# Kernel optimization log

Hardware: AMD Instinct MI355X
Metric: run time of the kernel (lower is better)

## Reference

```python
import jax, jax.numpy as jnp
import numpy as np

N_EMBD = 2048
N_HEAD = 16
N_KV_HEAD = 4
HD = N_EMBD // N_HEAD  # 128
B, T = 1, 4096
EPS = 1e-6


def apply_rope(x, cos, sin):
    # x: [B,T,H,hd]; cos/sin: [T,1,hd//2]
    hd = x.shape[-1] // 2
    x1, x2 = x[..., :hd], x[..., hd:]
    y1 = x1 * cos + x2 * sin
    y2 = x2 * cos - x1 * sin
    return jnp.concatenate((y1, y2), axis=-1).astype(x.dtype)


def rms_norm(x, eps=EPS):
    return x * jax.lax.rsqrt(jnp.mean(jnp.square(x), axis=-1, keepdims=True) + eps)


def setup_inputs() -> dict:
    key = jax.random.key(0)
    ks = jax.random.split(key, 7)
    s = 0.02
    return {
        "x": jax.random.normal(ks[0], (B, T, N_EMBD), dtype=jnp.float32),
        "cos": jax.random.normal(ks[1], (T, 1, HD // 2), dtype=jnp.float32),
        "sin": jax.random.normal(ks[2], (T, 1, HD // 2), dtype=jnp.float32),
        "wq": jax.random.normal(ks[3], (N_EMBD, N_HEAD * HD), dtype=jnp.float32) * s,
        "wk": jax.random.normal(ks[4], (N_EMBD, N_KV_HEAD * HD), dtype=jnp.float32) * s,
        "wv": jax.random.normal(ks[5], (N_EMBD, N_KV_HEAD * HD), dtype=jnp.float32) * s,
        "wo": jax.random.normal(ks[6], (N_EMBD, N_EMBD), dtype=jnp.float32) * s,
    }


def reference(x, cos, sin, wq, wk, wv, wo):
    Bb, Tt, C = x.shape
    q = (x @ wq).reshape(Bb, Tt, N_HEAD, HD)
    k = (x @ wk).reshape(Bb, Tt, N_KV_HEAD, HD)
    v = (x @ wv).reshape(Bb, Tt, N_KV_HEAD, HD)
    q = rms_norm(apply_rope(q, cos, sin))
    k = rms_norm(apply_rope(k, cos, sin))
    g = N_HEAD // N_KV_HEAD
    if g > 1:
        k = jnp.repeat(k, g, axis=2)  # [B,T,H,hd]
        v = jnp.repeat(v, g, axis=2)
    scale = 1.0 / jnp.sqrt(jnp.float32(HD))
    # scores: [B,H,T,S]
    scores = jnp.einsum("bthd,bshd->bhts", q, k) * scale
    causal = jnp.tril(jnp.ones((Tt, Tt), dtype=bool))
    scores = jnp.where(causal, scores, jnp.finfo(scores.dtype).min)
    attn = jax.nn.softmax(scores, axis=-1)
    y = jnp.einsum("bhts,bshd->bthd", attn, v).reshape(Bb, Tt, C)
    return y @ wo
```

## Files before the change

kernel.cpp:

```cpp
#include <hip/hip_runtime.h>

#define T_SEQ 4096
#define C_EMB 2048
#define NH 16
#define NKV 4
#define HD 128

typedef short bf16x8 __attribute__((ext_vector_type(8)));
typedef float f32x4 __attribute__((ext_vector_type(4)));
typedef unsigned short u16x4 __attribute__((ext_vector_type(4)));

__device__ inline unsigned short f2bf(float f) {
    unsigned int u = __float_as_uint(f);
    unsigned int r = (u + 0x7FFFu + ((u >> 16) & 1u)) >> 16;
    return (unsigned short)r;
}

__device__ __forceinline__ void async_cp16(const unsigned short* g, unsigned short* l) {
    __builtin_amdgcn_global_load_lds((const __attribute__((address_space(1))) unsigned int*)g,
                                     (__attribute__((address_space(3))) unsigned int*)l,
                                     16, 0, 0);
}

__global__ __launch_bounds__(256) void cvt_bf16(const float* __restrict__ in,
                                                unsigned short* __restrict__ out, int n) {
    int i = (blockIdx.x * 256 + threadIdx.x) * 4;
    if (i >= n) return;
    float4 f = *(const float4*)(&in[i]);
    u16x4 o;
    o.x = f2bf(f.x); o.y = f2bf(f.y); o.z = f2bf(f.z); o.w = f2bf(f.w);
    *(u16x4*)(&out[i]) = o;
}

__global__ __launch_bounds__(256) void transpose_all(const float* __restrict__ wq,
                                                     const float* __restrict__ wk,
                                                     const float* __restrict__ wv,
                                                     const float* __restrict__ wo,
                                                     unsigned short* __restrict__ wqkvT,
                                                     unsigned short* __restrict__ woT) {
    __shared__ float tile[32][33];
    int z = blockIdx.z;
    const float* in;
    unsigned short* out;
    int ld_in;
    if (z == 0)      { in = wq; out = wqkvT;                         ld_in = 2048; }
    else if (z == 1) { in = wk; out = wqkvT + (size_t)2048 * 2048;   ld_in = 512;  }
    else if (z == 2) { in = wv; out = wqkvT + (size_t)2560 * 2048;   ld_in = 512;  }
    else             { in = wo; out = woT;                           ld_in = 2048; }
    if ((z == 1 || z == 2) && blockIdx.x >= 16) return;

    int x = blockIdx.x * 32 + threadIdx.x;
    for (int i = threadIdx.y; i < 32; i += 8) {
        int y = blockIdx.y * 32 + i;
        tile[i][threadIdx.x] = in[(size_t)y * ld_in + x];
    }
    __syncthreads();
    int xo = blockIdx.y * 32 + threadIdx.x;
    for (int i = threadIdx.y; i < 32; i += 8) {
        int yo = blockIdx.x * 32 + i;
        out[(size_t)yo * 2048 + xo] = f2bf(tile[threadIdx.x][i]);
    }
}

__global__ __launch_bounds__(256, 3) void gemm_qkv(const unsigned short* __restrict__ A,
                                                   const unsigned short* __restrict__ Bt,
                                                   const float* __restrict__ cosb,
                                                   const float* __restrict__ sinb,
                                                   unsigned short* __restrict__ Qn,
                                                   unsigned short* __restrict__ Kn,
                                                   unsigned short* __restrict__ Vt) {
    __shared__ __align__(16) unsigned short As[3][128 * 32];
    __shared__ __align__(16) unsigned short Bs[3][128 * 32];
    const int K = 2048;
    int t = threadIdx.x;
    int w = t >> 6, lane = t & 63;
    int ln = lane & 15, q = lane >> 4;
    int wm = w * 32;

    int d = blockIdx.y * 24 + blockIdx.x;
    int xcd = d & 7, l = d >> 3;
    int lx = l % 12, ly = l / 12;
    int bx = (xcd & 1) * 12 + lx;
    int by = (xcd >> 1) * 8 + ly;
    int m0 = by * 128, n0 = bx * 128;

    f32x4 acc[2][8] = {};

    int r0 = t >> 2, c0 = (t & 3) ^ ((t >> 4) & 3);
    int L1 = 256 + t;
    int r1 = L1 >> 2, c1 = (L1 & 3) ^ ((L1 >> 4) & 3);
    const unsigned short* a0 = &A[(size_t)(m0 + r0) * K + c0 * 8];
    const unsigned short* a1 = &A[(size_t)(m0 + r1) * K + c1 * 8];
    const unsigned short* b0 = &Bt[(size_t)(n0 + r0) * K + c0 * 8];
    const unsigned short* b1 = &Bt[(size_t)(n0 + r1) * K + c1 * 8];

    auto stage = [&](int b, int k0) {
        async_cp16(a0 + k0, &As[b][w * 512]);
        async_cp16(a1 + k0, &As[b][2048 + w * 512]);
        async_cp16(b0 + k0, &Bs[b][w * 512]);
        async_cp16(b1 + k0, &Bs[b][2048 + w * 512]);
    };

    stage(0, 0);
    stage(1, 32);

    int bc = 0;
    for (int it = 0; it < 64; ++it) {
        if (it < 63) asm volatile("s_waitcnt vmcnt(4)" ::: "memory");
        else         asm volatile("s_waitcnt vmcnt(0)" ::: "memory");
        __builtin_amdgcn_s_barrier();
        __builtin_amdgcn_sched_barrier(0);
        if (it < 62) {
            int bn = bc + 2; if (bn >= 3) bn -= 3;
            stage(bn, (it + 2) * 32);
        }
        int cs = (q ^ ((ln >> 2) & 3)) * 8;
        bf16x8 af[2], bfr[8];
#pragma unroll
        for (int i = 0; i < 2; ++i) af[i] = *(const bf16x8*)(&As[bc][(wm + i * 16 + ln) * 32 + cs]);
#pragma unroll
        for (int j = 0; j < 8; ++j) bfr[j] = *(const bf16x8*)(&Bs[bc][(j * 16 + ln) * 32 + cs]);
#pragma unroll
        for (int i = 0; i < 2; ++i)
#pragma unroll
            for (int j = 0; j < 8; ++j)
                acc[i][j] = __builtin_amdgcn_mfma_f32_16x16x32_bf16(af[i], bfr[j], acc[i][j], 0, 0, 0);
        bc = (bc == 2) ? 0 : bc + 1;
    }

    if (n0 < 2560) {
        bool isQ = (n0 < 2048);
        int h = isQ ? (n0 >> 7) : ((n0 - 2048) >> 7);
#pragma unroll
        for (int i = 0; i < 2; ++i)
#pragma unroll
            for (int r = 0; r < 4; ++r) {
                int row = m0 + wm + i * 16 + q * 4 + r;
                float y1[4], y2[4];
                float ss = 0.0f;
#pragma unroll
                for (int j = 0; j < 4; ++j) {
                    float a = acc[i][j][r];
                    float b = acc[i][j + 4][r];
                    float cc = cosb[row * 64 + j * 16 + ln];
                    float sv = sinb[row * 64 + j * 16 + ln];
                    y1[j] = a * cc + b * sv;
                    y2[j] = b * cc - a * sv;
                    ss += y1[j] * y1[j] + y2[j] * y2[j];
                }
                ss += __shfl_xor(ss, 1);
                ss += __shfl_xor(ss, 2);
                ss += __shfl_xor(ss, 4);
                ss += __shfl_xor(ss, 8);
                float rv = rsqrtf(ss * (1.0f / 128.0f) + 1e-6f);
                if (isQ) {
                    float s = rv * (0.08838834764831845f * 1.4426950408889634f);
                    unsigned short* ob = Qn + (size_t)row * 2048 + h * 128;
#pragma unroll
                    for (int j = 0; j < 4; ++j) {
                        ob[j * 16 + ln] = f2bf(y1[j] * s);
                        ob[64 + j * 16 + ln] = f2bf(y2[j] * s);
                    }
                } else {
                    unsigned short* ob = Kn + (size_t)row * 512 + h * 128;
#pragma unroll
                    for (int j = 0; j < 4; ++j) {
                        ob[j * 16 + ln] = f2bf(y1[j] * rv);
                        ob[64 + j * 16 + ln] = f2bf(y2[j] * rv);
                    }
                }
            }
    } else {
        int v0 = n0 - 2560;
        unsigned short* sm = &As[0][0];
#pragma unroll
        for (int half = 0; half < 2; ++half) {
            __syncthreads();
#pragma unroll
            for (int i = 0; i < 2; ++i)
#pragma unroll
                for (int jj = 0; jj < 4; ++jj) {
                    int j = half * 4 + jj;
                    int cc = jj * 16 + ln;
                    int rr = wm + i * 16 + q * 4;
                    u16x4 pk;
                    pk.x = f2bf(acc[i][j][0]); pk.y = f2bf(acc[i][j][1]);
                    pk.z = f2bf(acc[i][j][2]); pk.w = f2bf(acc[i][j][3]);
                    *(u16x4*)(&sm[cc * 136 + rr]) = pk;
                }
            __syncthreads();
            int vtr = t >> 2, mseg = (t & 3) * 32;
            unsigned short* dst = Vt + (size_t)(v0 + half * 64 + vtr) * 4096 + m0 + mseg;
            const unsigned short* src = &sm[vtr * 136 + mseg];
            *(int4*)(dst)      = *(const int4*)(src);
            *(int4*)(dst + 8)  = *(const int4*)(src + 8);
            *(int4*)(dst + 16) = *(const int4*)(src + 16);
            *(int4*)(dst + 24) = *(const int4*)(src + 24);
        }
    }
}

__global__ __launch_bounds__(512, 2) void gemm_bt_v12(const unsigned short* __restrict__ A,
                                                      const unsigned short* __restrict__ Bt,
                                                      float* __restrict__ C, int M, int N, int K) {
    __shared__ __align__(16) unsigned short As[2][256 * 64];
    __shared__ __align__(16) unsigned short Bs[2][128 * 64];
    int t = threadIdx.x;
    int w = t >> 6, lane = t & 63;
    int ln = lane & 15, q = lane >> 4;
    int wr = w >> 1, wc = w & 1;
    int m0 = blockIdx.y * 256, n0 = blockIdx.x * 128;

    f32x4 acc[4][4] = {};

    const unsigned short* ab[4];
    const unsigned short* bb[2];
#pragma unroll
    for (int s = 0; s < 4; ++s) {
        int L = s * 512 + t;
        int r = L >> 3;
        int c = (L & 7) ^ (r & 7);
        ab[s] = &A[(size_t)(m0 + r) * K + c * 8];
    }
#pragma unroll
    for (int s = 0; s < 2; ++s) {
        int L = s * 512 + t;
        int r = L >> 3;
        int c = (L & 7) ^ (r & 7);
        bb[s] = &Bt[(size_t)(n0 + r) * K + c * 8];
    }

    auto stage = [&](int b, int k0) {
#pragma unroll
        for (int s = 0; s < 4; ++s) async_cp16(ab[s] + k0, &As[b][s * 4096 + w * 512]);
#pragma unroll
        for (int s = 0; s < 2; ++s) async_cp16(bb[s] + k0, &Bs[b][s * 4096 + w * 512]);
    };

    stage(0, 0);
    asm volatile("s_waitcnt vmcnt(0)" ::: "memory");
    __builtin_amdgcn_s_barrier();

    int buf = 0;
    for (int it = 0; it < 32; ++it) {
        if (it < 31) stage(buf ^ 1, (it + 1) * 64);
#pragma unroll
        for (int kk = 0; kk < 2; ++kk) {
            bf16x8 bfr[4];
#pragma unroll
            for (int j = 0; j < 4; ++j) {
                int row = wc * 64 + j * 16 + ln;
                bfr[j] = *(const bf16x8*)(&Bs[buf][row * 64 + (((kk * 4 + q) ^ (row & 7)) * 8)]);
            }
#pragma unroll
            for (int i = 0; i < 4; ++i) {
                int row = wr * 64 + i * 16 + ln;
                bf16x8 a = *(const bf16x8*)(&As[buf][row * 64 + (((kk * 4 + q) ^ (row & 7)) * 8)]);
#pragma unroll
                for (int j = 0; j < 4; ++j)
                    acc[i][j] = __builtin_amdgcn_mfma_f32_16x16x32_bf16(a, bfr[j], acc[i][j], 0, 0, 0);
            }
        }
        asm volatile("s_waitcnt vmcnt(0)" ::: "memory");
        __builtin_amdgcn_s_barrier();
        buf ^= 1;
    }

#pragma unroll
    for (int i = 0; i < 4; ++i)
#pragma unroll
        for (int j = 0; j < 4; ++j)
#pragma unroll
            for (int r = 0; r < 4; ++r) {
                int row = m0 + wr * 64 + i * 16 + q * 4 + r;
                int col = n0 + wc * 64 + j * 16 + ln;
                C[(size_t)row * N + col] = acc[i][j][r];
            }
}

__global__ __launch_bounds__(256) void flash_attn(const unsigned short* __restrict__ Qn,
                                                  const unsigned short* __restrict__ Kn,
                                                  const unsigned short* __restrict__ Vt,
                                                  unsigned short* __restrict__ Ao) {
    __shared__ __align__(16) unsigned short Ks[2][64 * 128];
    __shared__ __align__(16) unsigned short Vs[2][128 * 64];
    __shared__ __align__(16) unsigned short Pl[4][16 * 72];

    int pairi = blockIdx.x;
    int h = blockIdx.y;
    int kvh = h >> 2;
    int t = threadIdx.x;
    int w = t >> 6, lane = t & 63;
    int ln = lane & 15, q = lane >> 4;

    int nA = 64 - pairi;
    int bq = 63 - pairi;
    int wq0 = bq * 64 + w * 16;

    bf16x8 qf[4];
    {
        const unsigned short* qb = Qn + (size_t)(wq0 + ln) * 2048 + h * 128;
#pragma unroll
        for (int kc = 0; kc < 4; ++kc) qf[kc] = *(const bf16x8*)(qb + kc * 32 + q * 8);
    }

    f32x4 o[8] = {};
    f32x4 l_p = {0.f, 0.f, 0.f, 0.f};

    const unsigned short* kbase[4];
    const unsigned short* vbase[4];
#pragma unroll
    for (int s = 0; s < 4; ++s) {
        int L = s * 256 + t;
        int key = L >> 4;
        int ck = (L & 15) ^ (key & 15);
        kbase[s] = Kn + (size_t)key * 512 + kvh * 128 + ck * 8;
        int hd = L >> 3;
        int cv = (L & 7) ^ (hd & 7);
        vbase[s] = Vt + (size_t)(kvh * 128 + hd) * 4096 + cv * 8;
    }

#pragma unroll
    for (int s = 0; s < 4; ++s) async_cp16(kbase[s], &Ks[0][s * 2048 + w * 512]);
#pragma unroll
    for (int s = 0; s < 4; ++s) async_cp16(vbase[s], &Vs[0][s * 2048 + w * 512]);

    for (int it = 0; it < 65; ++it) {
        __syncthreads();

        int nxt = it + 1;
        if (nxt < 65) {
            int nkt = (nxt < nA) ? nxt * 64 : (nxt - nA) * 64;
            size_t koff = (size_t)nkt * 512;
            unsigned short* kd = Ks[nxt & 1];
            unsigned short* vd = Vs[nxt & 1];
#pragma unroll
            for (int s = 0; s < 4; ++s) async_cp16(kbase[s] + koff, kd + s * 2048 + w * 512);
#pragma unroll
            for (int s = 0; s < 4; ++s) async_cp16(vbase[s] + nkt, vd + s * 2048 + w * 512);
        }

        if (it == nA) {
#pragma unroll
            for (int r = 0; r < 4; ++r) {
                float lsum = l_p[r];
                lsum += __shfl_xor(lsum, 1);
                lsum += __shfl_xor(lsum, 2);
                lsum += __shfl_xor(lsum, 4);
                lsum += __shfl_xor(lsum, 8);
                float inv = 1.0f / lsum;
                int row = wq0 + q * 4 + r;
                unsigned short* ob = Ao + (size_t)row * 2048 + h * 128;
#pragma unroll
                for (int f = 0; f < 8; ++f) ob[f * 16 + ln] = f2bf(o[f][r] * inv);
            }
            bq = pairi;
            wq0 = bq * 64 + w * 16;
            const unsigned short* qb = Qn + (size_t)(wq0 + ln) * 2048 + h * 128;
#pragma unroll
            for (int kc = 0; kc < 4; ++kc) qf[kc] = *(const bf16x8*)(qb + kc * 32 + q * 8);
#pragma unroll
            for (int f = 0; f < 8; ++f) o[f] = (f32x4){0.f, 0.f, 0.f, 0.f};
            l_p = (f32x4){0.f, 0.f, 0.f, 0.f};
        }

        int kt0 = (it < nA) ? it * 64 : (it - nA) * 64;
        const unsigned short* kb = Ks[it & 1];
        const unsigned short* vb = Vs[it & 1];

        f32x4 sA[4] = {{-16.6f, -16.6f, -16.6f, -16.6f}, {-16.6f, -16.6f, -16.6f, -16.6f},
                       {-16.6f, -16.6f, -16.6f, -16.6f}, {-16.6f, -16.6f, -16.6f, -16.6f}};
        __builtin_amdgcn_s_setprio(1);
#pragma unroll
        for (int jt = 0; jt < 4; ++jt) {
            int key = jt * 16 + ln;
#pragma unroll
            for (int kc = 0; kc < 4; ++kc) {
                int cs = ((kc * 4 + q) ^ ln) * 8;
                bf16x8 kf = *(const bf16x8*)(&kb[key * 128 + cs]);
                sA[jt] = __builtin_amdgcn_mfma_f32_16x16x32_bf16(qf[kc], kf, sA[jt], 0, 0, 0);
            }
        }
        __builtin_amdgcn_s_setprio(0);
        if (kt0 + 63 > wq0) {
#pragma unroll
            for (int jt = 0; jt < 4; ++jt)
#pragma unroll
                for (int r = 0; r < 4; ++r) {
                    int key = kt0 + jt * 16 + ln;
                    int row = wq0 + q * 4 + r;
                    if (key > row) sA[jt][r] = -3e38f;
                }
        }
#pragma unroll
        for (int r = 0; r < 4; ++r) {
            int prow = (q * 4 + r) * 72;
#pragma unroll
            for (int jt = 0; jt < 4; ++jt) {
                float p = __builtin_amdgcn_exp2f(sA[jt][r]);
                Pl[w][prow + jt * 16 + ln] = (unsigned short)(__float_as_uint(p) >> 16);
                l_p[r] += p;
            }
        }

        __builtin_amdgcn_s_setprio(1);
#pragma unroll
        for (int ks = 0; ks < 2; ++ks) {
            bf16x8 pa = *(const bf16x8*)(&Pl[w][ln * 72 + ks * 32 + q * 8]);
            int cs = ((ks * 4 + q) ^ (ln & 7)) * 8;
#pragma unroll
            for (int f = 0; f < 8; ++f) {
                bf16x8 vf = *(const bf16x8*)(&vb[(f * 16 + ln) * 64 + cs]);
                o[f] = __builtin_amdgcn_mfma_f32_16x16x32_bf16(pa, vf, o[f], 0, 0, 0);
            }
        }
        __builtin_amdgcn_s_setprio(0);
    }
#pragma unroll
    for (int r = 0; r < 4; ++r) {
        float lsum = l_p[r];
        lsum += __shfl_xor(lsum, 1);
        lsum += __shfl_xor(lsum, 2);
        lsum += __shfl_xor(lsum, 4);
        lsum += __shfl_xor(lsum, 8);
        float inv = 1.0f / lsum;
        int row = wq0 + q * 4 + r;
        unsigned short* ob = Ao + (size_t)row * 2048 + h * 128;
#pragma unroll
        for (int f = 0; f < 8; ++f) ob[f * 16 + ln] = f2bf(o[f][r] * inv);
    }
}

extern "C" void kernel_launch(void* const* d_in, const int* in_sizes, int n_in,
                              void* d_out, int out_size, void* d_ws, size_t ws_size,
                              hipStream_t stream) {
    const float* x    = (const float*)d_in[0];
    const float* cosb = (const float*)d_in[1];
    const float* sinb = (const float*)d_in[2];
    const float* wq   = (const float*)d_in[3];
    const float* wk   = (const float*)d_in[4];
    const float* wv   = (const float*)d_in[5];
    const float* wo   = (const float*)d_in[6];
    float* out = (float*)d_out;

    char* ws = (char*)d_ws;
    unsigned short* xb    = (unsigned short*)ws;
    unsigned short* wqkvT = xb    + (size_t)4096 * 2048;
    unsigned short* woT   = wqkvT + (size_t)3072 * 2048;
    unsigned short* Qn    = woT   + (size_t)2048 * 2048;
    unsigned short* Kn    = Qn    + (size_t)4096 * 2048;
    unsigned short* Vt    = Kn    + (size_t)4096 * 512;
    unsigned short* Ao    = Vt    + (size_t)512 * 4096;

    cvt_bf16<<<(4096 * 2048 / 4 + 255) / 256, 256, 0, stream>>>(x, xb, 4096 * 2048);
    transpose_all<<<dim3(64, 64, 4), dim3(32, 8), 0, stream>>>(wq, wk, wv, wo, wqkvT, woT);
    gemm_qkv<<<dim3(24, 32), 256, 0, stream>>>(xb, wqkvT, cosb, sinb, Qn, Kn, Vt);
    flash_attn<<<dim3(32, 16), 256, 0, stream>>>(Qn, Kn, Vt, Ao);
    gemm_bt_v12<<<dim3(16, 16), 512, 0, stream>>>(Ao, woT, out, 4096, 2048, 2048);
}
```

Baseline: 352.6 us.

## Split flash-attention warps into 2x2 query/key groups with cross-warp reduction

```diff
diff --git a/kernel.cpp b/kernel.cpp
--- a/kernel.cpp
+++ b/kernel.cpp
@@ -284,7 +284,8 @@
                                                   unsigned short* __restrict__ Ao) {
     __shared__ __align__(16) unsigned short Ks[2][64 * 128];
     __shared__ __align__(16) unsigned short Vs[2][128 * 64];
-    __shared__ __align__(16) unsigned short Pl[4][16 * 72];
+    __shared__ __align__(16) unsigned short Pl[4][32 * 40];
+    __shared__ float lsh[2][2][32];
 
     int pairi = blockIdx.x;
     int h = blockIdx.y;
@@ -292,20 +293,25 @@
     int t = threadIdx.x;
     int w = t >> 6, lane = t & 63;
     int ln = lane & 15, q = lane >> 4;
+    int qg = w >> 1, kg = w & 1;
 
     int nA = 64 - pairi;
     int bq = 63 - pairi;
-    int wq0 = bq * 64 + w * 16;
-
-    bf16x8 qf[4];
+    int wq0 = bq * 64;
+
+    bf16x8 qf[2][4];
     {
-        const unsigned short* qb = Qn + (size_t)(wq0 + ln) * 2048 + h * 128;
-#pragma unroll
-        for (int kc = 0; kc < 4; ++kc) qf[kc] = *(const bf16x8*)(qb + kc * 32 + q * 8);
-    }
-
-    f32x4 o[8] = {};
-    f32x4 l_p = {0.f, 0.f, 0.f, 0.f};
+        const unsigned short* qb0 = Qn + (size_t)(wq0 + qg * 32 + ln) * 2048 + h * 128;
+        const unsigned short* qb1 = Qn + (size_t)(wq0 + qg * 32 + 16 + ln) * 2048 + h * 128;
+#pragma unroll
+        for (int kc = 0; kc < 4; ++kc) {
+            qf[0][kc] = *(const bf16x8*)(qb0 + kc * 32 + q * 8);
+            qf[1][kc] = *(const bf16x8*)(qb1 + kc * 32 + q * 8);
+        }
+    }
+
+    f32x4 o[2][8] = {};
+    f32x4 l_p[2] = {};
 
     const unsigned short* kbase[4];
     const unsigned short* vbase[4];
@@ -329,6 +335,61 @@
         __syncthreads();
 
         int nxt = it + 1;
+
+        if (it == nA) {
+            int fb = nxt & 1;
+            float* osh = (qg == 0) ? (float*)&Ks[fb][0] : (float*)&Vs[fb][0];
+            int nb = (kg ^ 1) * 4;
+#pragma unroll
+            for (int qi = 0; qi < 2; ++qi)
+#pragma unroll
+                for (int fi = 0; fi < 4; ++fi)
+#pragma unroll
+                    for (int r = 0; r < 4; ++r)
+                        osh[kg * 2048 + ((qi * 4 + fi) * 4 + r) * 64 + lane] = o[qi][nb + fi][r];
+            float l_red[2][4];
+#pragma unroll
+            for (int qi = 0; qi < 2; ++qi)
+#pragma unroll
+                for (int r = 0; r < 4; ++r) {
+                    float s = l_p[qi][r];
+                    s += __shfl_xor(s, 1); s += __shfl_xor(s, 2);
+                    s += __shfl_xor(s, 4); s += __shfl_xor(s, 8);
+                    l_red[qi][r] = s;
+                    if (ln == 0) lsh[qg][kg][qi * 16 + q * 4 + r] = s;
+                }
+            __syncthreads();
+#pragma unroll
+            for (int qi = 0; qi < 2; ++qi)
+#pragma unroll
+                for (int r = 0; r < 4; ++r) {
+                    float inv = 1.0f / (l_red[qi][r] + lsh[qg][kg ^ 1][qi * 16 + q * 4 + r]);
+                    int row = wq0 + qg * 32 + qi * 16 + q * 4 + r;
+                    unsigned short* ob = Ao + (size_t)row * 2048 + h * 128;
+#pragma unroll
+                    for (int fi = 0; fi < 4; ++fi) {
+                        int f = kg * 4 + fi;
+                        float v = o[qi][f][r] + osh[(kg ^ 1) * 2048 + ((qi * 4 + fi) * 4 + r) * 64 + lane];
+                        ob[f * 16 + ln] = f2bf(v * inv);
+                    }
+                }
+            __syncthreads();
+            bq = pairi; wq0 = bq * 64;
+            const unsigned short* qb0 = Qn + (size_t)(wq0 + qg * 32 + ln) * 2048 + h * 128;
+            const unsigned short* qb1 = Qn + (size_t)(wq0 + qg * 32 + 16 + ln) * 2048 + h * 128;
+#pragma unroll
+            for (int kc = 0; kc < 4; ++kc) {
+                qf[0][kc] = *(const bf16x8*)(qb0 + kc * 32 + q * 8);
+                qf[1][kc] = *(const bf16x8*)(qb1 + kc * 32 + q * 8);
+            }
+#pragma unroll
+            for (int qi = 0; qi < 2; ++qi) {
+#pragma unroll
+                for (int f = 0; f < 8; ++f) o[qi][f] = (f32x4){0.f, 0.f, 0.f, 0.f};
+                l_p[qi] = (f32x4){0.f, 0.f, 0.f, 0.f};
+            }
+        }
+
         if (nxt < 65) {
             int nkt = (nxt < nA) ? nxt * 64 : (nxt - nA) * 64;
             size_t koff = (size_t)nkt * 512;
@@ -340,94 +401,105 @@
             for (int s = 0; s < 4; ++s) async_cp16(vbase[s] + nkt, vd + s * 2048 + w * 512);
         }
 
-        if (it == nA) {
-#pragma unroll
-            for (int r = 0; r < 4; ++r) {
-                float lsum = l_p[r];
-                lsum += __shfl_xor(lsum, 1);
-                lsum += __shfl_xor(lsum, 2);
-                lsum += __shfl_xor(lsum, 4);
-                lsum += __shfl_xor(lsum, 8);
-                float inv = 1.0f / lsum;
-                int row = wq0 + q * 4 + r;
-                unsigned short* ob = Ao + (size_t)row * 2048 + h * 128;
-#pragma unroll
-                for (int f = 0; f < 8; ++f) ob[f * 16 + ln] = f2bf(o[f][r] * inv);
-            }
-            bq = pairi;
-            wq0 = bq * 64 + w * 16;
-            const unsigned short* qb = Qn + (size_t)(wq0 + ln) * 2048 + h * 128;
-#pragma unroll
-            for (int kc = 0; kc < 4; ++kc) qf[kc] = *(const bf16x8*)(qb + kc * 32 + q * 8);
-#pragma unroll
-            for (int f = 0; f < 8; ++f) o[f] = (f32x4){0.f, 0.f, 0.f, 0.f};
-            l_p = (f32x4){0.f, 0.f, 0.f, 0.f};
-        }
-
         int kt0 = (it < nA) ? it * 64 : (it - nA) * 64;
         const unsigned short* kb = Ks[it & 1];
         const unsigned short* vb = Vs[it & 1];
 
-        f32x4 sA[4] = {{-16.6f, -16.6f, -16.6f, -16.6f}, {-16.6f, -16.6f, -16.6f, -16.6f},
-                       {-16.6f, -16.6f, -16.6f, -16.6f}, {-16.6f, -16.6f, -16.6f, -16.6f}};
+        f32x4 sA[2][2];
+#pragma unroll
+        for (int qi = 0; qi < 2; ++qi)
+#pragma unroll
+            for (int kj = 0; kj < 2; ++kj)
+                sA[qi][kj] = (f32x4){-16.6f, -16.6f, -16.6f, -16.6f};
+
         __builtin_amdgcn_s_setprio(1);
 #pragma unroll
-        for (int jt = 0; jt < 4; ++jt) {
-            int key = jt * 16 + ln;
+        for (int kj = 0; kj < 2; ++kj) {
+            int key = kg * 32 + kj * 16 + ln;
 #pragma unroll
             for (int kc = 0; kc < 4; ++kc) {
-                int cs = ((kc * 4 + q) ^ ln) * 8;
-                bf16x8 kf = *(const bf16x8*)(&kb[key * 128 + cs]);
-                sA[jt] = __builtin_amdgcn_mfma_f32_16x16x32_bf16(qf[kc], kf, sA[jt], 0, 0, 0);
+                bf16x8 kf = *(const bf16x8*)(&kb[key * 128 + (((kc * 4 + q) ^ ln) * 8)]);
+                sA[0][kj] = __builtin_amdgcn_mfma_f32_16x16x32_bf16(qf[0][kc], kf, sA[0][kj], 0, 0, 0);
+                sA[1][kj] = __builtin_amdgcn_mfma_f32_16x16x32_bf16(qf[1][kc], kf, sA[1][kj], 0, 0, 0);
             }
         }
         __builtin_amdgcn_s_setprio(0);
-        if (kt0 + 63 > wq0) {
-#pragma unroll
-            for (int jt = 0; jt < 4; ++jt)
-#pragma unroll
-                for (int r = 0; r < 4; ++r) {
-                    int key = kt0 + jt * 16 + ln;
-                    int row = wq0 + q * 4 + r;
-                    if (key > row) sA[jt][r] = -3e38f;
-                }
-        }
-#pragma unroll
-        for (int r = 0; r < 4; ++r) {
-            int prow = (q * 4 + r) * 72;
-#pragma unroll
-            for (int jt = 0; jt < 4; ++jt) {
-                float p = __builtin_amdgcn_exp2f(sA[jt][r]);
-                Pl[w][prow + jt * 16 + ln] = (unsigned short)(__float_as_uint(p) >> 16);
-                l_p[r] += p;
-            }
-        }
-
+
+        if (kt0 + kg * 32 + 31 > wq0 + qg * 32) {
+#pragma unroll
+            for (int qi = 0; qi < 2; ++qi)
+#pragma unroll
+                for (int kj = 0; kj < 2; ++kj)
+#pragma unroll
+                    for (int r = 0; r < 4; ++r) {
+                        int key = kt0 + kg * 32 + kj * 16 + ln;
+                        int row = wq0 + qg * 32 + qi * 16 + q * 4 + r;
+                        if (key > row) sA[qi][kj][r] = -3e38f;
+                    }
+        }
+
+#pragma unroll
+        for (int qi = 0; qi < 2; ++qi)
+#pragma unroll
+            for (int r = 0; r < 4; ++r) {
+                int prow = (qi * 16 + q * 4 + r) * 40;
+#pragma unroll
+                for (int kj = 0; kj < 2; ++kj) {
+                    float p = __builtin_amdgcn_exp2f(sA[qi][kj][r]);
+                    Pl[w][prow + kj * 16 + ln] = (unsigned short)(__float_as_uint(p) >> 16);
+                    l_p[qi][r] += p;
+                }
+            }
+
+        bf16x8 pa0 = *(const bf16x8*)(&Pl[w][ln * 40 + q * 8]);
+        bf16x8 pa1 = *(const bf16x8*)(&Pl[w][(16 + ln) * 40 + q * 8]);
         __builtin_amdgcn_s_setprio(1);
 #pragma unroll
-        for (int ks = 0; ks < 2; ++ks) {
-            bf16x8 pa = *(const bf16x8*)(&Pl[w][ln * 72 + ks * 32 + q * 8]);
-            int cs = ((ks * 4 + q) ^ (ln & 7)) * 8;
-#pragma unroll
-            for (int f = 0; f < 8; ++f) {
-                bf16x8 vf = *(const bf16x8*)(&vb[(f * 16 + ln) * 64 + cs]);
-                o[f] = __builtin_amdgcn_mfma_f32_16x16x32_bf16(pa, vf, o[f], 0, 0, 0);
-            }
+        for (int f = 0; f < 8; ++f) {
+            bf16x8 vf = *(const bf16x8*)(&vb[(f * 16 + ln) * 64 + (((kg * 4 + q) ^ (ln & 7)) * 8)]);
+            o[0][f] = __builtin_amdgcn_mfma_f32_16x16x32_bf16(pa0, vf, o[0][f], 0, 0, 0);
+            o[1][f] = __builtin_amdgcn_mfma_f32_16x16x32_bf16(pa1, vf, o[1][f], 0, 0, 0);
         }
         __builtin_amdgcn_s_setprio(0);
     }
-#pragma unroll
-    for (int r = 0; r < 4; ++r) {
-        float lsum = l_p[r];
-        lsum += __shfl_xor(lsum, 1);
-        lsum += __shfl_xor(lsum, 2);
-        lsum += __shfl_xor(lsum, 4);
-        lsum += __shfl_xor(lsum, 8);
-        float inv = 1.0f / lsum;
-        int row = wq0 + q * 4 + r;
-        unsigned short* ob = Ao + (size_t)row * 2048 + h * 128;
-#pragma unroll
-        for (int f = 0; f < 8; ++f) ob[f * 16 + ln] = f2bf(o[f][r] * inv);
+
+    {
+        int fb = 1;
+        float* osh = (qg == 0) ? (float*)&Ks[fb][0] : (float*)&Vs[fb][0];
+        int nb = (kg ^ 1) * 4;
+#pragma unroll
+        for (int qi = 0; qi < 2; ++qi)
+#pragma unroll
+            for (int fi = 0; fi < 4; ++fi)
+#pragma unroll
+                for (int r = 0; r < 4; ++r)
+                    osh[kg * 2048 + ((qi * 4 + fi) * 4 + r) * 64 + lane] = o[qi][nb + fi][r];
+        float l_red[2][4];
+#pragma unroll
+        for (int qi = 0; qi < 2; ++qi)
+#pragma unroll
+            for (int r = 0; r < 4; ++r) {
+                float s = l_p[qi][r];
+                s += __shfl_xor(s, 1); s += __shfl_xor(s, 2);
+                s += __shfl_xor(s, 4); s += __shfl_xor(s, 8);
+                l_red[qi][r] = s;
+                if (ln == 0) lsh[qg][kg][qi * 16 + q * 4 + r] = s;
+            }
+        __syncthreads();
+#pragma unroll
+        for (int qi = 0; qi < 2; ++qi)
+#pragma unroll
+            for (int r = 0; r < 4; ++r) {
+                float inv = 1.0f / (l_red[qi][r] + lsh[qg][kg ^ 1][qi * 16 + q * 4 + r]);
+                int row = wq0 + qg * 32 + qi * 16 + q * 4 + r;
+                unsigned short* ob = Ao + (size_t)row * 2048 + h * 128;
+#pragma unroll
+                for (int fi = 0; fi < 4; ++fi) {
+                    int f = kg * 4 + fi;
+                    float v = o[qi][f][r] + osh[(kg ^ 1) * 2048 + ((qi * 4 + fi) * 4 + r) * 64 + lane];
+                    ob[f * 16 + ln] = f2bf(v * inv);
+                }
+            }
     }
 }
 
```

Result: slower. 814.6 us (+131.0%).
